# Performance work log

Hardware: AMD Instinct MI355X
Metric: run time of the kernel (lower is better)

The kernel has to match this reference:

```python
import jax, jax.numpy as jnp
import numpy as np

N, S, K, H, D = 8192, 16384, 16, 8, 512
E = N * K
HEAD_DIM = D // H


def setup_inputs() -> dict:
    key = jax.random.key(0)
    ks = jax.random.split(key, 12)
    x = jax.random.normal(ks[0], (N, D), jnp.float32)
    # every destination row gets K edges so softmax rows are never empty
    row_index = jnp.repeat(jnp.arange(N, dtype=jnp.int32), K)  # [E], sorted
    src_index = jax.random.randint(ks[1], (E,), 0, S, dtype=jnp.int32)
    att_bias = jax.random.normal(ks[2], (H, E), jnp.float32)
    dist = jax.random.uniform(ks[3], (E,), jnp.float32, minval=0.5, maxval=10.0)
    pos = jax.random.normal(ks[4], (N, 3), jnp.float32)
    src_pos = jax.random.normal(ks[5], (S, 3), jnp.float32)
    org_to_src = jax.random.randint(ks[6], (S,), 0, N, dtype=jnp.int32)
    scale = 1.0 / np.sqrt(D).astype(np.float32)
    Wq = jax.random.normal(ks[7], (D, D), jnp.float32) * scale
    bq = jax.random.normal(ks[8], (D,), jnp.float32) * 0.01
    Wk = jax.random.normal(ks[9], (D, D), jnp.float32) * scale
    bk = jax.random.normal(ks[10], (D,), jnp.float32) * 0.01
    return {"x": x, "row_index": row_index, "src_index": src_index,
            "att_bias": att_bias, "dist": dist, "pos": pos, "src_pos": src_pos,
            "org_to_src": org_to_src, "Wq": Wq, "bq": bq, "Wk": Wk, "bk": bk}


def reference(x, row_index, src_index, att_bias, dist, pos, src_pos, org_to_src,
              Wq, bq, Wk, bk):
    n, d_model = x.shape
    h, e = att_bias.shape
    hd = d_model // h
    # Projections -> [N, H, hd]; key gathered to the source list via org_to_src -> [S, H, hd]
    q = (x @ Wq + bq).reshape(n, h, hd)
    k_src = ((x @ Wk + bk).reshape(n, h, hd))[org_to_src]
    # Per-edge masked logits: (q/sqrt(hd)) . k + att_bias   (COO sparse attention)
    q_e = q[row_index]                       # [E, H, hd]
    k_e = k_src[src_index]                   # [E, H, hd]
    logits = jnp.einsum('ehd,ehd->eh', q_e, k_e) / np.sqrt(hd).astype(np.float32)
    logits = logits + att_bias.T             # [E, H]
    # Segment softmax over edges sharing a destination row
    m = jax.ops.segment_max(logits, row_index, num_segments=n)      # [N, H]
    p = jnp.exp(logits - m[row_index])
    z = jax.ops.segment_sum(p, row_index, num_segments=n)           # [N, H]
    att = p / z[row_index]                                          # [E, H]
    # Distance reweighting: 1/dist with dist==0 -> 0 weight
    safe = jnp.where(dist == 0, 1.0, dist)
    inv_d = jnp.where(dist == 0, 0.0, 1.0 / safe)
    att = att * inv_d[:, None]
    # dst_vec = att @ src_pos ; src_vec = (att @ 1) * pos   (both as segment sums)
    dst = jax.ops.segment_sum(att[:, :, None] * src_pos[src_index][:, None, :],
                              row_index, num_segments=n)            # [N, H, 3]
    asum = jax.ops.segment_sum(att, row_index, num_segments=n)      # [N, H]
    feat = dst - asum[:, :, None] * pos[:, None, :]                 # [N, H, 3]
    return feat.reshape(n, h * 3)
```

## Files before the change

kernel.cpp:

```cpp
#include <hip/hip_runtime.h>

#define N_ROWS 8192
#define D_MODEL 512
#define KT 512
#define NC 1024
#define NHEAD 8
#define KEDGE 16
#define NEDGE (N_ROWS * KEDGE)
#define BK 64

using f32x4  = __attribute__((ext_vector_type(4))) float;
using bf16x8 = __attribute__((ext_vector_type(8))) __bf16;
using u16x8  = __attribute__((ext_vector_type(8))) unsigned short;

__device__ __forceinline__ unsigned short bf16_rtne(float f) {
    unsigned u = __float_as_uint(f);
    u += 0x7FFFu + ((u >> 16) & 1u);
    return (unsigned short)(u >> 16);
}
__device__ __forceinline__ float from_bf16(unsigned short b) {
    return __uint_as_float(((unsigned)b) << 16);
}

#define GLOAD16(gp, lp) __builtin_amdgcn_global_load_lds( \
    (__attribute__((address_space(1))) void*)(void*)(gp), \
    (__attribute__((address_space(3))) void*)(lp), 16, 0, 0)

__global__ __launch_bounds__(256) void prep(const float* __restrict__ x,
                                            const float* __restrict__ Wq,
                                            const float* __restrict__ Wk,
                                            const int* __restrict__ src_index,
                                            const int* __restrict__ org_to_src,
                                            const float* __restrict__ att_bias,
                                            const float* __restrict__ dist,
                                            const float* __restrict__ src_pos,
                                            unsigned short* __restrict__ Xb,
                                            unsigned short* __restrict__ Bt,
                                            int* __restrict__ KN,
                                            float4* __restrict__ Rec,
                                            float* __restrict__ AtT) {
    if (blockIdx.x < 2048) {
        const int i = (blockIdx.x * 256 + threadIdx.x) * 8;
        const float4 a = *reinterpret_cast<const float4*>(x + i);
        const float4 b = *reinterpret_cast<const float4*>(x + i + 4);
        u16x8 o;
        o[0] = bf16_rtne(a.x); o[1] = bf16_rtne(a.y);
        o[2] = bf16_rtne(a.z); o[3] = bf16_rtne(a.w);
        o[4] = bf16_rtne(b.x); o[5] = bf16_rtne(b.y);
        o[6] = bf16_rtne(b.z); o[7] = bf16_rtne(b.w);
        *reinterpret_cast<u16x8*>(Xb + i) = o;
    } else if (blockIdx.x < 4096) {
        const int gid = (blockIdx.x - 2048) * 256 + threadIdx.x;
        const int j = gid >> 9;
        const int k = gid & 511;
        const float* W = (j < 512) ? Wq : Wk;
        Bt[(size_t)j * KT + k] = bf16_rtne(W[k * D_MODEL + (j & 511)]);
    } else {
        const int ge = (blockIdx.x - 4096) * 256 + threadIdx.x;
        const int s = src_index[ge];
        KN[ge] = org_to_src[s];
        const float d = dist[ge];
        float4 r;
        r.x = src_pos[s * 3 + 0];
        r.y = src_pos[s * 3 + 1];
        r.z = src_pos[s * 3 + 2];
        r.w = (d == 0.f) ? 0.f : 1.f / d;
        Rec[ge] = r;
        float4 b0, b1;
        b0.x = att_bias[0 * (size_t)NEDGE + ge];
        b0.y = att_bias[1 * (size_t)NEDGE + ge];
        b0.z = att_bias[2 * (size_t)NEDGE + ge];
        b0.w = att_bias[3 * (size_t)NEDGE + ge];
        b1.x = att_bias[4 * (size_t)NEDGE + ge];
        b1.y = att_bias[5 * (size_t)NEDGE + ge];
        b1.z = att_bias[6 * (size_t)NEDGE + ge];
        b1.w = att_bias[7 * (size_t)NEDGE + ge];
        *reinterpret_cast<float4*>(AtT + (size_t)ge * 8)     = b0;
        *reinterpret_cast<float4*>(AtT + (size_t)ge * 8 + 4) = b1;
    }
}

__global__ __launch_bounds__(512) void gemm_qk(
    const unsigned short* __restrict__ Xb, const unsigned short* __restrict__ Bt,
    const float* __restrict__ bq, const float* __restrict__ bk,
    unsigned short* __restrict__ Qp, unsigned short* __restrict__ Kp)
{
    __shared__ __align__(16) unsigned short As[2][128 * BK];
    __shared__ __align__(16) unsigned short Bs[2][128 * BK];

    const int tid  = threadIdx.x;
    const int lane = tid & 63;
    const int wave = tid >> 6;
    const int wr   = wave >> 2;
    const int wc   = wave & 3;

    const int bid = blockIdx.x;
    const int xcd = bid & 7;
    const int j   = bid >> 3;
    const int rp  = xcd * 8 + (j >> 3);
    const int cp  = j & 7;
    const int row0 = rp * 128, col0 = cp * 128;

    f32x4 acc[4][2];
    #pragma unroll
    for (int m = 0; m < 4; ++m)
        #pragma unroll
        for (int n = 0; n < 2; ++n)
            acc[m][n] = (f32x4){0.f, 0.f, 0.f, 0.f};

    const int crow = tid >> 3;
    const int sc   = ((tid & 7) ^ (crow & 7)) * 8;

    const unsigned short* gA = Xb + (size_t)(row0 + crow) * D_MODEL + sc;
    const unsigned short* gB = Bt + (size_t)(col0 + crow) * KT     + sc;

    #define STAGE(b, kb) do { \
        GLOAD16(gA + (kb),                &As[b][tid * 8]); \
        GLOAD16(gA + (kb) + 64 * D_MODEL, &As[b][(tid + 512) * 8]); \
        GLOAD16(gB + (kb),                &Bs[b][tid * 8]); \
        GLOAD16(gB + (kb) + 64 * KT,      &Bs[b][(tid + 512) * 8]); \
    } while (0)

    STAGE(0, 0);
    __syncthreads();

    int buf = 0;
    for (int kt = 0; kt < KT / BK; ++kt) {
        if (kt < KT / BK - 1) STAGE(buf ^ 1, (kt + 1) * BK);
        #pragma unroll
        for (int kk = 0; kk < 2; ++kk) {
            const int kc = kk * 4 + (lane >> 4);
            bf16x8 afr[4], bfr[2];
            #pragma unroll
            for (int m = 0; m < 4; ++m) {
                const int r = wr * 64 + m * 16 + (lane & 15);
                afr[m] = __builtin_bit_cast(bf16x8, *reinterpret_cast<const u16x8*>(
                    &As[buf][r * BK + ((kc ^ (r & 7)) * 8)]));
            }
            #pragma unroll
            for (int n = 0; n < 2; ++n) {
                const int r = wc * 32 + n * 16 + (lane & 15);
                bfr[n] = __builtin_bit_cast(bf16x8, *reinterpret_cast<const u16x8*>(
                    &Bs[buf][r * BK + ((kc ^ (r & 7)) * 8)]));
            }
            #pragma unroll
            for (int m = 0; m < 4; ++m)
                #pragma unroll
                for (int n = 0; n < 2; ++n)
                    acc[m][n] = __builtin_amdgcn_mfma_f32_16x16x32_bf16(
                        afr[m], bfr[n], acc[m][n], 0, 0, 0);
        }
        __syncthreads();
        buf ^= 1;
    }
    #undef STAGE

    #pragma unroll
    for (int m = 0; m < 4; ++m) {
        const int row = row0 + wr * 64 + m * 16 + (lane >> 4) * 4;
        #pragma unroll
        for (int n = 0; n < 2; ++n) {
            const int c = col0 + wc * 32 + n * 16 + (lane & 15);
            const int cc = c & 511;
            unsigned short* plane = (c < 512) ? Qp : Kp;
            const float bias = (c < 512) ? bq[cc] : bk[cc];
            #pragma unroll
            for (int r = 0; r < 4; ++r)
                plane[(size_t)(row + r) * D_MODEL + cc] = bf16_rtne(acc[m][n][r] + bias);
        }
    }
}

__global__ __launch_bounds__(256) void edge_kernel(
    const unsigned short* __restrict__ Qp, const unsigned short* __restrict__ Kp,
    const int* __restrict__ KN,
    const float4* __restrict__ Rec,
    const float* __restrict__ AtT,
    const float* __restrict__ pos,
    float* __restrict__ out)
{
    const int lane = threadIdx.x & 63;
    const int wave = threadIdx.x >> 6;
    const int n = blockIdx.x * 4 + wave;
    const int ll = lane & 31;
    const int half = lane >> 5;
    const int h = ll >> 2;
    const int o1 = h * 64 + (ll & 3) * 8;
    const int o2 = o1 + 32;

    const u16x8 q1 = *reinterpret_cast<const u16x8*>(Qp + (size_t)n * D_MODEL + o1);
    const u16x8 q2 = *reinterpret_cast<const u16x8*>(Qp + (size_t)n * D_MODEL + o2);
    float qf1[8], qf2[8];
    #pragma unroll
    for (int i = 0; i < 8; ++i) { qf1[i] = from_bf16(q1[i]); qf2[i] = from_bf16(q2[i]); }

    int kne[8];
    #pragma unroll
    for (int i = 0; i < 8; ++i) kne[i] = KN[n * KEDGE + 2 * i + half];

    float logit[8];
    #pragma unroll
    for (int i = 0; i < 8; ++i) {
        const unsigned short* kp = Kp + (size_t)kne[i] * D_MODEL;
        const u16x8 k1 = *reinterpret_cast<const u16x8*>(kp + o1);
        const u16x8 k2 = *reinterpret_cast<const u16x8*>(kp + o2);
        float p = 0.f;
        #pragma unroll
        for (int jj = 0; jj < 8; ++jj)
            p += qf1[jj] * from_bf16(k1[jj]) + qf2[jj] * from_bf16(k2[jj]);
        p += __shfl_xor(p, 1);
        p += __shfl_xor(p, 2);
        logit[i] = p * 0.125f + AtT[(size_t)(n * KEDGE + 2 * i + half) * 8 + h];
    }

    float mx = logit[0];
    #pragma unroll
    for (int i = 1; i < 8; ++i) mx = fmaxf(mx, logit[i]);
    mx = fmaxf(mx, __shfl_xor(mx, 32));
    float pe[8];
    float z = 0.f;
    #pragma unroll
    for (int i = 0; i < 8; ++i) { pe[i] = __expf(logit[i] - mx); z += pe[i]; }
    z += __shfl_xor(z, 32);
    const float rz = 1.f / z;

    float d0 = 0.f, d1 = 0.f, d2 = 0.f, asum = 0.f;
    #pragma unroll
    for (int i = 0; i < 8; ++i) {
        const float4 r = Rec[n * KEDGE + 2 * i + half];
        const float w = pe[i] * rz * r.w;
        d0 += w * r.x; d1 += w * r.y; d2 += w * r.z;
        asum += w;
    }
    d0 += __shfl_xor(d0, 32);
    d1 += __shfl_xor(d1, 32);
    d2 += __shfl_xor(d2, 32);
    asum += __shfl_xor(asum, 32);

    const int c = ll & 3;
    if (half == 0 && c < 3) {
        const float dc = (c == 0) ? d0 : ((c == 1) ? d1 : d2);
        out[n * 24 + h * 3 + c] = dc - asum * pos[n * 3 + c];
    }
}

extern "C" void kernel_launch(void* const* d_in, const int* in_sizes, int n_in,
                              void* d_out, int out_size, void* d_ws, size_t ws_size,
                              hipStream_t stream) {
    const float* x          = (const float*)d_in[0];
    const int*   src_index  = (const int*)d_in[2];
    const float* att_bias   = (const float*)d_in[3];
    const float* dist       = (const float*)d_in[4];
    const float* pos        = (const float*)d_in[5];
    const float* src_pos    = (const float*)d_in[6];
    const int*   org_to_src = (const int*)d_in[7];
    const float* Wq         = (const float*)d_in[8];
    const float* bq         = (const float*)d_in[9];
    const float* Wk         = (const float*)d_in[10];
    const float* bk         = (const float*)d_in[11];
    float* out = (float*)d_out;

    char* ws = (char*)d_ws;
    unsigned short* Xb  = (unsigned short*)(ws);
    unsigned short* Bt  = (unsigned short*)(ws + ( 8u << 20));
    unsigned short* Qp  = (unsigned short*)(ws + ( 9u << 20));
    unsigned short* Kp  = (unsigned short*)(ws + (17u << 20));
    int*            KN  = (int*)           (ws + (25u << 20));
    float4*         Rec = (float4*)        (ws + (26u << 20));
    float*          AtT = (float*)         (ws + (28u << 20));

    prep<<<dim3(4608), dim3(256), 0, stream>>>(
        x, Wq, Wk, src_index, org_to_src, att_bias, dist, src_pos,
        Xb, Bt, KN, Rec, AtT);
    gemm_qk<<<dim3(512), dim3(512), 0, stream>>>(Xb, Bt, bq, bk, Qp, Kp);
    edge_kernel<<<dim3(N_ROWS / 4), dim3(256), 0, stream>>>(
        Qp, Kp, KN, Rec, AtT, pos, out);
}
```

Before: 44.39 us.

## Pre-swizzle operands into MFMA fragment layout and drop LDS staging in GEMM

The prep kernel now writes x and the weight matrices in bf16, already arranged in MFMA fragment order, so each lane can load its 16-byte fragment straight from global memory. The GEMM drops LDS double-buffering and barriers in favour of register ping-pong prefetch, with 4 waves each computing a 64x64 tile (4x4 MFMAs). Weight conversion now packs 8 values per thread, so prep launches fewer blocks. The cost is that L2 replaces LDS for operand reuse across waves, and the strided weight reads in prep are uncoalesced.

```diff
diff --git a/kernel.cpp b/kernel.cpp
--- a/kernel.cpp
+++ b/kernel.cpp
@@ -3,11 +3,10 @@
 #define N_ROWS 8192
 #define D_MODEL 512
 #define KT 512
-#define NC 1024
+#define KTC 16
 #define NHEAD 8
 #define KEDGE 16
 #define NEDGE (N_ROWS * KEDGE)
-#define BK 64
 
 using f32x4  = __attribute__((ext_vector_type(4))) float;
 using bf16x8 = __attribute__((ext_vector_type(8))) __bf16;
@@ -21,10 +20,6 @@
 __device__ __forceinline__ float from_bf16(unsigned short b) {
     return __uint_as_float(((unsigned)b) << 16);
 }
-
-#define GLOAD16(gp, lp) __builtin_amdgcn_global_load_lds( \
-    (__attribute__((address_space(1))) void*)(void*)(gp), \
-    (__attribute__((address_space(3))) void*)(lp), 16, 0, 0)
 
 __global__ __launch_bounds__(256) void prep(const float* __restrict__ x,
                                             const float* __restrict__ Wq,
@@ -34,29 +29,40 @@
                                             const float* __restrict__ att_bias,
                                             const float* __restrict__ dist,
                                             const float* __restrict__ src_pos,
-                                            unsigned short* __restrict__ Xb,
-                                            unsigned short* __restrict__ Bt,
+                                            unsigned short* __restrict__ AF,
+                                            unsigned short* __restrict__ BF,
                                             int* __restrict__ KN,
                                             float4* __restrict__ Rec,
                                             float* __restrict__ AtT) {
     if (blockIdx.x < 2048) {
-        const int i = (blockIdx.x * 256 + threadIdx.x) * 8;
-        const float4 a = *reinterpret_cast<const float4*>(x + i);
-        const float4 b = *reinterpret_cast<const float4*>(x + i + 4);
+        const int gid = blockIdx.x * 256 + threadIdx.x;
+        const int lane = gid & 63;
+        const int fid = gid >> 6;
+        const int row = (fid >> 4) * 16 + (lane & 15);
+        const int k0  = (fid & 15) * 32 + (lane >> 4) * 8;
+        const float4 a = *reinterpret_cast<const float4*>(x + (size_t)row * D_MODEL + k0);
+        const float4 b = *reinterpret_cast<const float4*>(x + (size_t)row * D_MODEL + k0 + 4);
         u16x8 o;
         o[0] = bf16_rtne(a.x); o[1] = bf16_rtne(a.y);
         o[2] = bf16_rtne(a.z); o[3] = bf16_rtne(a.w);
         o[4] = bf16_rtne(b.x); o[5] = bf16_rtne(b.y);
         o[6] = bf16_rtne(b.z); o[7] = bf16_rtne(b.w);
-        *reinterpret_cast<u16x8*>(Xb + i) = o;
-    } else if (blockIdx.x < 4096) {
+        *reinterpret_cast<u16x8*>(AF + (size_t)gid * 8) = o;
+    } else if (blockIdx.x < 2304) {
         const int gid = (blockIdx.x - 2048) * 256 + threadIdx.x;
-        const int j = gid >> 9;
-        const int k = gid & 511;
-        const float* W = (j < 512) ? Wq : Wk;
-        Bt[(size_t)j * KT + k] = bf16_rtne(W[k * D_MODEL + (j & 511)]);
+        const int lane = gid & 63;
+        const int fid = gid >> 6;
+        const int c  = (fid >> 4) * 16 + (lane & 15);
+        const int k0 = (fid & 15) * 32 + (lane >> 4) * 8;
+        const float* W = (c < 512) ? Wq : Wk;
+        const int cc = c & 511;
+        u16x8 o;
+        #pragma unroll
+        for (int j = 0; j < 8; ++j)
+            o[j] = bf16_rtne(W[(size_t)(k0 + j) * D_MODEL + cc]);
+        *reinterpret_cast<u16x8*>(BF + (size_t)gid * 8) = o;
     } else {
-        const int ge = (blockIdx.x - 4096) * 256 + threadIdx.x;
+        const int ge = (blockIdx.x - 2304) * 256 + threadIdx.x;
         const int s = src_index[ge];
         KN[ge] = org_to_src[s];
         const float d = dist[ge];
@@ -80,93 +86,76 @@
     }
 }
 
-__global__ __launch_bounds__(512) void gemm_qk(
-    const unsigned short* __restrict__ Xb, const unsigned short* __restrict__ Bt,
+__global__ __launch_bounds__(256) void gemm_qk(
+    const unsigned short* __restrict__ AF, const unsigned short* __restrict__ BF,
     const float* __restrict__ bq, const float* __restrict__ bk,
     unsigned short* __restrict__ Qp, unsigned short* __restrict__ Kp)
 {
-    __shared__ __align__(16) unsigned short As[2][128 * BK];
-    __shared__ __align__(16) unsigned short Bs[2][128 * BK];
-
     const int tid  = threadIdx.x;
     const int lane = tid & 63;
-    const int wave = tid >> 6;
-    const int wr   = wave >> 2;
-    const int wc   = wave & 3;
-
-    const int bid = blockIdx.x;
-    const int xcd = bid & 7;
-    const int j   = bid >> 3;
-    const int rp  = xcd * 8 + (j >> 3);
-    const int cp  = j & 7;
-    const int row0 = rp * 128, col0 = cp * 128;
-
-    f32x4 acc[4][2];
+    const int w    = tid >> 6;
+    const int b    = blockIdx.x;
+    const int xcd  = b & 7;
+    const int r    = b >> 3;
+    const int bct  = xcd * 2 + (r & 1);
+    const int brt  = r >> 1;
+    const int rt0  = brt * 16 + w * 4;
+    const int ct0  = bct * 4;
+
+    const unsigned short* pa = AF + (size_t)rt0 * KTC * 512 + lane * 8;
+    const unsigned short* pb = BF + (size_t)ct0 * KTC * 512 + lane * 8;
+
+    f32x4 acc[4][4];
     #pragma unroll
     for (int m = 0; m < 4; ++m)
         #pragma unroll
-        for (int n = 0; n < 2; ++n)
+        for (int n = 0; n < 4; ++n)
             acc[m][n] = (f32x4){0.f, 0.f, 0.f, 0.f};
 
-    const int crow = tid >> 3;
-    const int sc   = ((tid & 7) ^ (crow & 7)) * 8;
-
-    const unsigned short* gA = Xb + (size_t)(row0 + crow) * D_MODEL + sc;
-    const unsigned short* gB = Bt + (size_t)(col0 + crow) * KT     + sc;
-
-    #define STAGE(b, kb) do { \
-        GLOAD16(gA + (kb),                &As[b][tid * 8]); \
-        GLOAD16(gA + (kb) + 64 * D_MODEL, &As[b][(tid + 512) * 8]); \
-        GLOAD16(gB + (kb),                &Bs[b][tid * 8]); \
-        GLOAD16(gB + (kb) + 64 * KT,      &Bs[b][(tid + 512) * 8]); \
-    } while (0)
-
-    STAGE(0, 0);
-    __syncthreads();
-
-    int buf = 0;
-    for (int kt = 0; kt < KT / BK; ++kt) {
-        if (kt < KT / BK - 1) STAGE(buf ^ 1, (kt + 1) * BK);
-        #pragma unroll
-        for (int kk = 0; kk < 2; ++kk) {
-            const int kc = kk * 4 + (lane >> 4);
-            bf16x8 afr[4], bfr[2];
-            #pragma unroll
-            for (int m = 0; m < 4; ++m) {
-                const int r = wr * 64 + m * 16 + (lane & 15);
-                afr[m] = __builtin_bit_cast(bf16x8, *reinterpret_cast<const u16x8*>(
-                    &As[buf][r * BK + ((kc ^ (r & 7)) * 8)]));
-            }
-            #pragma unroll
-            for (int n = 0; n < 2; ++n) {
-                const int r = wc * 32 + n * 16 + (lane & 15);
-                bfr[n] = __builtin_bit_cast(bf16x8, *reinterpret_cast<const u16x8*>(
-                    &Bs[buf][r * BK + ((kc ^ (r & 7)) * 8)]));
-            }
-            #pragma unroll
-            for (int m = 0; m < 4; ++m)
-                #pragma unroll
-                for (int n = 0; n < 2; ++n)
-                    acc[m][n] = __builtin_amdgcn_mfma_f32_16x16x32_bf16(
-                        afr[m], bfr[n], acc[m][n], 0, 0, 0);
-        }
-        __syncthreads();
-        buf ^= 1;
-    }
-    #undef STAGE
+    u16x8 aE[4], bE[4], aO[4], bO[4];
+
+#define LOADF(A_, B_, kt_) do { \
+    _Pragma("unroll") \
+    for (int m = 0; m < 4; ++m) \
+        A_[m] = *reinterpret_cast<const u16x8*>(pa + ((size_t)m * KTC + (kt_)) * 512); \
+    _Pragma("unroll") \
+    for (int n = 0; n < 4; ++n) \
+        B_[n] = *reinterpret_cast<const u16x8*>(pb + ((size_t)n * KTC + (kt_)) * 512); \
+} while (0)
+
+#define MFMA16(A_, B_) do { \
+    _Pragma("unroll") \
+    for (int m = 0; m < 4; ++m) \
+        _Pragma("unroll") \
+        for (int n = 0; n < 4; ++n) \
+            acc[m][n] = __builtin_amdgcn_mfma_f32_16x16x32_bf16( \
+                __builtin_bit_cast(bf16x8, A_[m]), __builtin_bit_cast(bf16x8, B_[n]), \
+                acc[m][n], 0, 0, 0); \
+} while (0)
+
+    LOADF(aE, bE, 0);
+    #pragma unroll
+    for (int kt = 0; kt < KTC; kt += 2) {
+        LOADF(aO, bO, kt + 1);
+        MFMA16(aE, bE);
+        if (kt + 2 < KTC) LOADF(aE, bE, kt + 2);
+        MFMA16(aO, bO);
+    }
+#undef LOADF
+#undef MFMA16
 
     #pragma unroll
     for (int m = 0; m < 4; ++m) {
-        const int row = row0 + wr * 64 + m * 16 + (lane >> 4) * 4;
-        #pragma unroll
-        for (int n = 0; n < 2; ++n) {
-            const int c = col0 + wc * 32 + n * 16 + (lane & 15);
+        const int row = brt * 256 + w * 64 + m * 16 + (lane >> 4) * 4;
+        #pragma unroll
+        for (int n = 0; n < 4; ++n) {
+            const int c = bct * 64 + n * 16 + (lane & 15);
             const int cc = c & 511;
             unsigned short* plane = (c < 512) ? Qp : Kp;
             const float bias = (c < 512) ? bq[cc] : bk[cc];
             #pragma unroll
-            for (int r = 0; r < 4; ++r)
-                plane[(size_t)(row + r) * D_MODEL + cc] = bf16_rtne(acc[m][n][r] + bias);
+            for (int rr = 0; rr < 4; ++rr)
+                plane[(size_t)(row + rr) * D_MODEL + cc] = bf16_rtne(acc[m][n][rr] + bias);
         }
     }
 }
@@ -227,10 +216,10 @@
     float d0 = 0.f, d1 = 0.f, d2 = 0.f, asum = 0.f;
     #pragma unroll
     for (int i = 0; i < 8; ++i) {
-        const float4 r = Rec[n * KEDGE + 2 * i + half];
-        const float w = pe[i] * rz * r.w;
-        d0 += w * r.x; d1 += w * r.y; d2 += w * r.z;
-        asum += w;
+        const float4 rr = Rec[n * KEDGE + 2 * i + half];
+        const float wgt = pe[i] * rz * rr.w;
+        d0 += wgt * rr.x; d1 += wgt * rr.y; d2 += wgt * rr.z;
+        asum += wgt;
     }
     d0 += __shfl_xor(d0, 32);
     d1 += __shfl_xor(d1, 32);
@@ -261,18 +250,18 @@
     float* out = (float*)d_out;
 
     char* ws = (char*)d_ws;
-    unsigned short* Xb  = (unsigned short*)(ws);
-    unsigned short* Bt  = (unsigned short*)(ws + ( 8u << 20));
+    unsigned short* AF  = (unsigned short*)(ws);
+    unsigned short* BF  = (unsigned short*)(ws + ( 8u << 20));
     unsigned short* Qp  = (unsigned short*)(ws + ( 9u << 20));
     unsigned short* Kp  = (unsigned short*)(ws + (17u << 20));
     int*            KN  = (int*)           (ws + (25u << 20));
     float4*         Rec = (float4*)        (ws + (26u << 20));
     float*          AtT = (float*)         (ws + (28u << 20));
 
-    prep<<<dim3(4608), dim3(256), 0, stream>>>(
+    prep<<<dim3(2816), dim3(256), 0, stream>>>(
         x, Wq, Wk, src_index, org_to_src, att_bias, dist, src_pos,
-        Xb, Bt, KN, Rec, AtT);
-    gemm_qk<<<dim3(512), dim3(512), 0, stream>>>(Xb, Bt, bq, bk, Qp, Kp);
+        AF, BF, KN, Rec, AtT);
+    gemm_qk<<<dim3(512), dim3(256), 0, stream>>>(AF, BF, bq, bk, Qp, Kp);
     edge_kernel<<<dim3(N_ROWS / 4), dim3(256), 0, stream>>>(
         Qp, Kp, KN, Rec, AtT, pos, out);
 }
```

Measured after the change: 45.21 us (median of 2 runs). About the same (+1.8%).
